# Kernel optimization log

Hardware: AMD Instinct MI355X
Metric: run time of the kernel (lower is better)

Reference implementation:

```python
import jax, jax.numpy as jnp
import numpy as np

B, N, C = 64, 1024, 128
H1, H2 = 256, 128
ACTION = N


def _xavier(key, shape):
    lim = float(np.sqrt(6.0 / (shape[0] + shape[1])))
    return jax.random.uniform(key, shape, jnp.float32, -lim, lim)


def setup_inputs() -> dict:
    key = jax.random.key(0)
    ks = jax.random.split(key, 16)
    node_features = jax.random.normal(ks[0], (B, N, 3), jnp.float32)
    adjacency_matrix = jax.random.randint(ks[1], (B, N, N), 0, 2).astype(jnp.int32)
    return {
        "node_features": node_features,
        "adjacency_matrix": adjacency_matrix,
        "W_in": _xavier(ks[2], (3, C)),
        "a_src": _xavier(ks[3], (C, 1)),
        "a_dst": _xavier(ks[4], (C, 1)),
        "a_src2": _xavier(ks[5], (C, 1)),
        "a_dst2": _xavier(ks[6], (C, 1)),
        "W1": _xavier(ks[7], (C, H1)),
        "b1": jnp.zeros((H1,), jnp.float32),
        "W2": _xavier(ks[8], (H1, H2)),
        "b2": jnp.zeros((H2,), jnp.float32),
        "Wpi": _xavier(ks[9], (H2, ACTION)),
        "bpi": jnp.zeros((ACTION,), jnp.float32),
        "Wv": _xavier(ks[10], (H2, 1)),
        "bv": jnp.zeros((1,), jnp.float32),
    }


def _gat_layer(x, mask, a_src, a_dst):
    # x: [B,N,C]; mask: [B,N,N] bool
    ai = jnp.squeeze(x @ a_src, -1)  # [B,N] score of node as source (i)
    aj = jnp.squeeze(x @ a_dst, -1)  # [B,N] score of node as dest (j)
    e = ai[:, :, None] + aj[:, None, :]  # [B,N,N]
    e = jnp.where(e > 0, e, 0.2 * e)  # leaky_relu(0.2)
    e = jnp.where(mask, e, jnp.float32(-1e9))  # masked_fill(-inf)
    alpha = jax.nn.softmax(e, axis=-1)  # [B,N,N]
    out = jnp.einsum("bij,bjc->bic", alpha, x)  # weighted neighbor aggregation
    return jax.nn.relu(out)


def reference(node_features, adjacency_matrix, W_in, a_src, a_dst, a_src2, a_dst2,
              W1, b1, W2, b2, Wpi, bpi, Wv, bv):
    mask = adjacency_matrix > 0
    x = node_features @ W_in  # [B,N,C], no bias
    x = _gat_layer(x, mask, a_src, a_dst)
    x = _gat_layer(x, mask, a_src2, a_dst2)
    x = jnp.mean(x, axis=1)  # [B,C]
    x = jax.nn.relu(x @ W1 + b1)
    x = jax.nn.relu(x @ W2 + b2)
    pi = jax.nn.softmax(x @ Wpi + bpi, axis=1)
    v = x @ Wv + bv
    return (pi, v)
```

## Files before the change

### kernel.cpp

```cpp
#include <hip/hip_runtime.h>

#define Bn 64
#define Nn 1024
#define Cc 128

typedef _Float16 h8 __attribute__((ext_vector_type(8)));
typedef float f4v __attribute__((ext_vector_type(4)));
typedef unsigned long long u64;

__global__ __launch_bounds__(256) void k_feat(
    const float* __restrict__ nf, const float* __restrict__ Win,
    const float* __restrict__ asrc, const float* __restrict__ adst,
    _Float16* __restrict__ X0, float* __restrict__ ai, float* __restrict__ aj,
    float* __restrict__ E, float* __restrict__ G, float* __restrict__ F, float* __restrict__ H) {
  int g = blockIdx.x; int b = g >> 7; int n0 = (g & 127) << 3;
  int t = threadIdx.x; int c = t >> 1; int h = t & 1;
  float w0 = Win[c], w1 = Win[Cc + c], w2 = Win[2 * Cc + c];
  float as_ = asrc[c], ad = adst[c];
  float ps[4], pd[4];
  _Float16 hv[4];
  #pragma unroll
  for (int r = 0; r < 4; r++) {
    int n = n0 + (h << 2) + r;
    const float* p = nf + ((size_t)(b << 10) + n) * 3;
    float x = p[0] * w0 + p[1] * w1 + p[2] * w2;
    hv[r] = (_Float16)x; ps[r] = x * as_; pd[r] = x * ad;
  }
  *(uint2*)(X0 + ((size_t)b << 17) + ((size_t)(g & 127) << 10) + (c << 3) + (h << 2)) = *(uint2*)hv;
  #pragma unroll
  for (int off = 32; off > 1; off >>= 1) {
    #pragma unroll
    for (int r = 0; r < 4; r++) { ps[r] += __shfl_down(ps[r], off, 64); pd[r] += __shfl_down(pd[r], off, 64); }
  }
  __shared__ float red[4][2][4][2];
  int lane = t & 63, wv = t >> 6;
  if (lane < 2) {
    #pragma unroll
    for (int r = 0; r < 4; r++) { red[wv][lane][r][0] = ps[r]; red[wv][lane][r][1] = pd[r]; }
  }
  __syncthreads();
  if (t < 8) {
    int hh = t >> 2, r = t & 3;
    float sa = 0.f, sd = 0.f;
    #pragma unroll
    for (int w = 0; w < 4; w++) { sa += red[w][hh][r][0]; sd += red[w][hh][r][1]; }
    int gi = (b << 10) + n0 + t;
    ai[gi] = sa; aj[gi] = sd;
    E[gi] = __expf(sa); G[gi] = __expf(0.2f * sa);
    F[gi] = __expf(sd); H[gi] = __expf(0.2f * sd);
  }
}

__global__ __launch_bounds__(256) void k_scores2(
    const _Float16* __restrict__ X1,
    const float* __restrict__ asrc, const float* __restrict__ adst,
    float* __restrict__ ai, float* __restrict__ aj,
    float* __restrict__ E, float* __restrict__ G, float* __restrict__ F, float* __restrict__ H) {
  int g = blockIdx.x; int b = g >> 7; int n0 = (g & 127) << 3;
  int t = threadIdx.x; int c = t >> 1; int h = t & 1;
  float as_ = asrc[c], ad = adst[c];
  uint2 raw = *(const uint2*)(X1 + ((size_t)b << 17) + ((size_t)(g & 127) << 10) + (c << 3) + (h << 2));
  const _Float16* hp = (const _Float16*)&raw;
  float ps[4], pd[4];
  #pragma unroll
  for (int r = 0; r < 4; r++) { float x = (float)hp[r]; ps[r] = x * as_; pd[r] = x * ad; }
  #pragma unroll
  for (int off = 32; off > 1; off >>= 1) {
    #pragma unroll
    for (int r = 0; r < 4; r++) { ps[r] += __shfl_down(ps[r], off, 64); pd[r] += __shfl_down(pd[r], off, 64); }
  }
  __shared__ float red[4][2][4][2];
  int lane = t & 63, wv = t >> 6;
  if (lane < 2) {
    #pragma unroll
    for (int r = 0; r < 4; r++) { red[wv][lane][r][0] = ps[r]; red[wv][lane][r][1] = pd[r]; }
  }
  __syncthreads();
  if (t < 8) {
    int hh = t >> 2, r = t & 3;
    float sa = 0.f, sd = 0.f;
    #pragma unroll
    for (int w = 0; w < 4; w++) { sa += red[w][hh][r][0]; sd += red[w][hh][r][1]; }
    int gi = (b << 10) + n0 + t;
    ai[gi] = sa; aj[gi] = sd;
    E[gi] = __expf(sa); G[gi] = __expf(0.2f * sa);
    F[gi] = __expf(sd); H[gi] = __expf(0.2f * sd);
  }
}

template <int LAYER>
__global__ __launch_bounds__(256, 3) void k_agg(
    const _Float16* __restrict__ X, const int* __restrict__ adj,
    const float* __restrict__ ai, const float* __restrict__ E, const float* __restrict__ G,
    const float* __restrict__ aj, const float* __restrict__ F, const float* __restrict__ H,
    u64* __restrict__ pm, _Float16* __restrict__ Y, float* __restrict__ xmp) {
  __shared__ __align__(16) char smem[24064];
  float* s_aj = (float*)smem;
  float* s_F  = (float*)(smem + 4096);
  float* s_H  = (float*)(smem + 8192);
  unsigned char* s_pm = (unsigned char*)(smem + 12288);
  float* s_col = (float*)(smem + 22016);

  const int b = blockIdx.y, i0 = blockIdx.x << 6;
  const int tid = threadIdx.x;
  const int lane = tid & 63, w = tid >> 6;
  const int m = lane & 15, quad = lane >> 4;
  const int gbase = b << 10;

  ((float4*)s_aj)[tid] = ((const float4*)(aj + gbase))[tid];
  ((float4*)s_F)[tid]  = ((const float4*)(F + gbase))[tid];
  ((float4*)s_H)[tid]  = ((const float4*)(H + gbase))[tid];

  if (LAYER == 1) {
    ushort* pmu = (ushort*)pm;
    #pragma unroll 2
    for (int pass = 0; pass < 16; ++pass) {
      int r = (w << 4) + pass;
      const uint4* arow = (const uint4*)(adj + ((size_t)(gbase + i0 + r) << 10));
      uint4 v0 = arow[(lane << 2) | 0], v1 = arow[(lane << 2) | 1];
      uint4 v2 = arow[(lane << 2) | 2], v3 = arow[(lane << 2) | 3];
      unsigned int bits =
          (v0.x) | (v0.y << 1) | (v0.z << 2) | (v0.w << 3) |
          (v1.x << 4) | (v1.y << 5) | (v1.z << 6) | (v1.w << 7) |
          (v2.x << 8) | (v2.y << 9) | (v2.z << 10) | (v2.w << 11) |
          (v3.x << 12) | (v3.y << 13) | (v3.z << 14) | (v3.w << 15);
      *(ushort*)(s_pm + r * 152 + (lane << 1)) = (ushort)bits;
      pmu[((size_t)(gbase + i0 + r) << 6) + lane] = (ushort)bits;
    }
  } else {
    const u64* pmg = pm + (((size_t)(gbase + i0)) << 4);
    #pragma unroll
    for (int k = tid; k < 1024; k += 256) {
      int r = k >> 4, wd = k & 15;
      *(u64*)(s_pm + r * 152 + (wd << 3)) = pmg[k];
    }
  }

  const int irow = (w << 4) + m;
  const int gi = gbase + i0 + irow;
  const float ai_i = ai[gi];
  const float Ed = E[gi], Gd = G[gi];
  float dsum = 0.f;

  f4v acc[8];
  #pragma unroll
  for (int ct = 0; ct < 8; ct++) { f4v z = {0.f, 0.f, 0.f, 0.f}; acc[ct] = z; }

  const h8* xb = (const h8*)(X + ((size_t)b << 17));
  const int prow = irow * 152;
  __syncthreads();

  for (int kt = 0; kt < 32; ++kt) {
    const h8* bsrc = xb + (kt << 9) + (quad << 7) + m;
    h8 bf0 = bsrc[0],  bf1 = bsrc[16], bf2 = bsrc[32],  bf3 = bsrc[48];
    h8 bf4 = bsrc[64], bf5 = bsrc[80], bf6 = bsrc[96],  bf7 = bsrc[112];
    const int j0 = (kt << 5) + (quad << 3);
    float aw[8], fw[8], hw[8];
    *(float4*)&aw[0] = *(const float4*)&s_aj[j0]; *(float4*)&aw[4] = *(const float4*)&s_aj[j0 + 4];
    *(float4*)&fw[0] = *(const float4*)&s_F[j0];  *(float4*)&fw[4] = *(const float4*)&s_F[j0 + 4];
    *(float4*)&hw[0] = *(const float4*)&s_H[j0];  *(float4*)&hw[4] = *(const float4*)&s_H[j0 + 4];
    unsigned int mb = s_pm[prow + (kt << 2) + quad];
    h8 af;
    #pragma unroll
    for (int jj = 0; jj < 8; jj++) {
      float e = ai_i + aw[jj];
      bool pos = e > 0.f;
      float wi_ = pos ? Ed : Gd;
      float wj_ = pos ? fw[jj] : hw[jj];
      float val = ((mb >> jj) & 1u) ? wi_ * wj_ : 0.f;
      dsum += val;
      af[jj] = (_Float16)val;
    }
    acc[0] = __builtin_amdgcn_mfma_f32_16x16x32_f16(af, bf0, acc[0], 0, 0, 0);
    acc[1] = __builtin_amdgcn_mfma_f32_16x16x32_f16(af, bf1, acc[1], 0, 0, 0);
    acc[2] = __builtin_amdgcn_mfma_f32_16x16x32_f16(af, bf2, acc[2], 0, 0, 0);
    acc[3] = __builtin_amdgcn_mfma_f32_16x16x32_f16(af, bf3, acc[3], 0, 0, 0);
    acc[4] = __builtin_amdgcn_mfma_f32_16x16x32_f16(af, bf4, acc[4], 0, 0, 0);
    acc[5] = __builtin_amdgcn_mfma_f32_16x16x32_f16(af, bf5, acc[5], 0, 0, 0);
    acc[6] = __builtin_amdgcn_mfma_f32_16x16x32_f16(af, bf6, acc[6], 0, 0, 0);
    acc[7] = __builtin_amdgcn_mfma_f32_16x16x32_f16(af, bf7, acc[7], 0, 0, 0);
  }

  dsum += __shfl_xor(dsum, 16, 64);
  dsum += __shfl_xor(dsum, 32, 64);
  float rd[4];
  #pragma unroll
  for (int r = 0; r < 4; r++) rd[r] = 1.0f / __shfl(dsum, (quad << 2) + r, 64);

  if (LAYER == 1) {
    const int g8 = ((i0 + (w << 4)) >> 3) + (quad >> 1);
    _Float16* yb = Y + ((size_t)b << 17) + (size_t)g8 * 1024 + ((quad & 1) << 2);
    #pragma unroll
    for (int ct = 0; ct < 8; ct++) {
      int c = (ct << 4) + m;
      _Float16 hv[4];
      #pragma unroll
      for (int r = 0; r < 4; r++) hv[r] = (_Float16)fmaxf(acc[ct][r] * rd[r], 0.f);
      *(uint2*)(yb + c * 8) = *(uint2*)hv;
    }
  } else {
    #pragma unroll
    for (int ct = 0; ct < 8; ct++) {
      float cs = (fmaxf(acc[ct][0] * rd[0], 0.f) + fmaxf(acc[ct][1] * rd[1], 0.f))
               + (fmaxf(acc[ct][2] * rd[2], 0.f) + fmaxf(acc[ct][3] * rd[3], 0.f));
      cs += __shfl_xor(cs, 16, 64);
      cs += __shfl_xor(cs, 32, 64);
      if (quad == 0) s_col[(w << 7) + (ct << 4) + m] = cs;
    }
    __syncthreads();
    if (tid < 128) {
      float s = s_col[tid] + s_col[128 + tid] + s_col[256 + tid] + s_col[384 + tid];
      xmp[(((b << 4) + blockIdx.x) << 7) + tid] = s;
    }
  }
}

__global__ __launch_bounds__(256) void k_head(
    const float* __restrict__ xmp, const float* __restrict__ W1, const float* __restrict__ b1,
    const float* __restrict__ W2, const float* __restrict__ b2,
    const float* __restrict__ Wpi, const float* __restrict__ bpi,
    const float* __restrict__ Wv, const float* __restrict__ bv,
    float* __restrict__ out) {
  int b = blockIdx.x, t = threadIdx.x;
  __shared__ float xs[128], h1[256], h2[128], red[4];
  if (t < 128) {
    const float* p = xmp + ((size_t)b << 11);
    float s = 0.f;
    #pragma unroll
    for (int xb = 0; xb < 16; xb++) s += p[(xb << 7) + t];
    xs[t] = s * (1.f / 1024.f);
  }
  __syncthreads();
  float s = 0.f;
  #pragma unroll 8
  for (int k = 0; k < 128; k++) s += xs[k] * W1[k * 256 + t];
  h1[t] = fmaxf(s + b1[t], 0.f);
  __syncthreads();
  if (t < 128) {
    float s2 = 0.f;
    #pragma unroll 8
    for (int k = 0; k < 256; k++) s2 += h1[k] * W2[k * 128 + t];
    h2[t] = fmaxf(s2 + b2[t], 0.f);
  }
  __syncthreads();
  float lg[4];
  #pragma unroll
  for (int q = 0; q < 4; q++) {
    int o = t + (q << 8);
    float s3 = 0.f;
    #pragma unroll 8
    for (int k = 0; k < 128; k++) s3 += h2[k] * Wpi[k * 1024 + o];
    lg[q] = s3 + bpi[o];
  }
  float mx = fmaxf(fmaxf(lg[0], lg[1]), fmaxf(lg[2], lg[3]));
  #pragma unroll
  for (int off = 32; off > 0; off >>= 1) mx = fmaxf(mx, __shfl_down(mx, off, 64));
  if ((t & 63) == 0) red[t >> 6] = mx;
  __syncthreads();
  mx = fmaxf(fmaxf(red[0], red[1]), fmaxf(red[2], red[3]));
  __syncthreads();
  float ex[4]; float sum = 0.f;
  #pragma unroll
  for (int q = 0; q < 4; q++) { ex[q] = __expf(lg[q] - mx); sum += ex[q]; }
  #pragma unroll
  for (int off = 32; off > 0; off >>= 1) sum += __shfl_down(sum, off, 64);
  if ((t & 63) == 0) red[t >> 6] = sum;
  __syncthreads();
  sum = red[0] + red[1] + red[2] + red[3];
  float rs = 1.0f / sum;
  #pragma unroll
  for (int q = 0; q < 4; q++) out[((size_t)b << 10) + t + (q << 8)] = ex[q] * rs;
  __syncthreads();
  float vp = (t < 128) ? h2[t] * Wv[t] : 0.f;
  #pragma unroll
  for (int off = 32; off > 0; off >>= 1) vp += __shfl_down(vp, off, 64);
  if ((t & 63) == 0) red[t >> 6] = vp;
  __syncthreads();
  if (t == 0) out[65536 + b] = red[0] + red[1] + red[2] + red[3] + bv[0];
}

extern "C" void kernel_launch(void* const* d_in, const int* in_sizes, int n_in,
                              void* d_out, int out_size, void* d_ws, size_t ws_size,
                              hipStream_t stream) {
  const float* nf    = (const float*)d_in[0];
  const int*   adj   = (const int*)  d_in[1];
  const float* Win   = (const float*)d_in[2];
  const float* asrc  = (const float*)d_in[3];
  const float* adst  = (const float*)d_in[4];
  const float* asrc2 = (const float*)d_in[5];
  const float* adst2 = (const float*)d_in[6];
  const float* W1    = (const float*)d_in[7];
  const float* b1    = (const float*)d_in[8];
  const float* W2    = (const float*)d_in[9];
  const float* b2    = (const float*)d_in[10];
  const float* Wpi   = (const float*)d_in[11];
  const float* bpi   = (const float*)d_in[12];
  const float* Wv    = (const float*)d_in[13];
  const float* bv    = (const float*)d_in[14];
  float* out = (float*)d_out;

  char* ws = (char*)d_ws;
  _Float16* x0 = (_Float16*)(ws);
  _Float16* x1 = (_Float16*)(ws + 16777216);
  u64* pm = (u64*)(ws + 33554432);
  char* S = ws + 41943040;
  float* ai1 = (float*)(S + 0 * 262144);
  float* aj1 = (float*)(S + 1 * 262144);
  float* E1  = (float*)(S + 2 * 262144);
  float* G1  = (float*)(S + 3 * 262144);
  float* F1  = (float*)(S + 4 * 262144);
  float* H1  = (float*)(S + 5 * 262144);
  float* ai2 = (float*)(S + 6 * 262144);
  float* aj2 = (float*)(S + 7 * 262144);
  float* E2  = (float*)(S + 8 * 262144);
  float* G2  = (float*)(S + 9 * 262144);
  float* F2  = (float*)(S + 10 * 262144);
  float* H2  = (float*)(S + 11 * 262144);
  float* xmp = (float*)(S + 12 * 262144);

  k_feat<<<8192, 256, 0, stream>>>(nf, Win, asrc, adst, x0, ai1, aj1, E1, G1, F1, H1);
  dim3 ag(16, Bn);
  k_agg<1><<<ag, 256, 0, stream>>>(x0, adj, ai1, E1, G1, aj1, F1, H1, pm, x1, nullptr);
  k_scores2<<<8192, 256, 0, stream>>>(x1, asrc2, adst2, ai2, aj2, E2, G2, F2, H2);
  k_agg<2><<<ag, 256, 0, stream>>>(x1, nullptr, ai2, E2, G2, aj2, F2, H2, pm, nullptr, xmp);
  k_head<<<Bn, 256, 0, stream>>>(xmp, W1, b1, W2, b2, Wpi, bpi, Wv, bv, out);
}
```

Baseline: 564.9 us.

## Fuse all stages into one cooperative persistent kernel with grid syncs

Replaces the five separate kernel launches with a single cooperative persistent kernel. Each stage runs as a grid-stride loop over its work items, and the stages are separated by grid.sync(). If the cooperative launch fails, the code falls back to the original five-launch sequence. The aim is to remove launch gaps and tail effects between stages. The cost is grid-wide barriers, reduced occupancy because the grid size comes from an occupancy query, and the loss of the launch_bounds(256,3) hint on the aggregation stage. The adjacency packing loop unroll also goes from 2 to 4.

```diff
diff --git a/kernel.cpp b/kernel.cpp
--- a/kernel.cpp
+++ b/kernel.cpp
@@ -1,4 +1,7 @@
 #include <hip/hip_runtime.h>
+#include <hip/hip_cooperative_groups.h>
+
+namespace cg = cooperative_groups;
 
 #define Bn 64
 #define Nn 1024
@@ -8,13 +11,28 @@
 typedef float f4v __attribute__((ext_vector_type(4)));
 typedef unsigned long long u64;
 
-__global__ __launch_bounds__(256) void k_feat(
-    const float* __restrict__ nf, const float* __restrict__ Win,
+struct Params {
+  const float* nf; const int* adj;
+  const float* Win; const float* asrc; const float* adst;
+  const float* asrc2; const float* adst2;
+  const float* W1; const float* b1; const float* W2; const float* b2;
+  const float* Wpi; const float* bpi; const float* Wv; const float* bv;
+  float* out;
+  _Float16* x0; _Float16* x1; u64* pm;
+  float* ai1; float* aj1; float* E1; float* G1; float* F1; float* H1;
+  float* ai2; float* aj2; float* E2; float* G2; float* F2; float* H2;
+  float* xmp;
+};
+
+__device__ __forceinline__ void feat_group(
+    int g, int t, const float* __restrict__ nf, const float* __restrict__ Win,
     const float* __restrict__ asrc, const float* __restrict__ adst,
     _Float16* __restrict__ X0, float* __restrict__ ai, float* __restrict__ aj,
-    float* __restrict__ E, float* __restrict__ G, float* __restrict__ F, float* __restrict__ H) {
-  int g = blockIdx.x; int b = g >> 7; int n0 = (g & 127) << 3;
-  int t = threadIdx.x; int c = t >> 1; int h = t & 1;
+    float* __restrict__ E, float* __restrict__ G, float* __restrict__ F, float* __restrict__ H,
+    char* smem) {
+  float (*red)[2][4][2] = (float(*)[2][4][2])smem;
+  int b = g >> 7; int n0 = (g & 127) << 3;
+  int c = t >> 1; int h = t & 1;
   float w0 = Win[c], w1 = Win[Cc + c], w2 = Win[2 * Cc + c];
   float as_ = asrc[c], ad = adst[c];
   float ps[4], pd[4];
@@ -32,7 +50,6 @@
     #pragma unroll
     for (int r = 0; r < 4; r++) { ps[r] += __shfl_down(ps[r], off, 64); pd[r] += __shfl_down(pd[r], off, 64); }
   }
-  __shared__ float red[4][2][4][2];
   int lane = t & 63, wv = t >> 6;
   if (lane < 2) {
     #pragma unroll
@@ -49,15 +66,18 @@
     E[gi] = __expf(sa); G[gi] = __expf(0.2f * sa);
     F[gi] = __expf(sd); H[gi] = __expf(0.2f * sd);
   }
-}
-
-__global__ __launch_bounds__(256) void k_scores2(
-    const _Float16* __restrict__ X1,
+  __syncthreads();
+}
+
+__device__ __forceinline__ void scores_group(
+    int g, int t, const _Float16* __restrict__ X1,
     const float* __restrict__ asrc, const float* __restrict__ adst,
     float* __restrict__ ai, float* __restrict__ aj,
-    float* __restrict__ E, float* __restrict__ G, float* __restrict__ F, float* __restrict__ H) {
-  int g = blockIdx.x; int b = g >> 7; int n0 = (g & 127) << 3;
-  int t = threadIdx.x; int c = t >> 1; int h = t & 1;
+    float* __restrict__ E, float* __restrict__ G, float* __restrict__ F, float* __restrict__ H,
+    char* smem) {
+  float (*red)[2][4][2] = (float(*)[2][4][2])smem;
+  int b = g >> 7; int n0 = (g & 127) << 3;
+  int c = t >> 1; int h = t & 1;
   float as_ = asrc[c], ad = adst[c];
   uint2 raw = *(const uint2*)(X1 + ((size_t)b << 17) + ((size_t)(g & 127) << 10) + (c << 3) + (h << 2));
   const _Float16* hp = (const _Float16*)&raw;
@@ -69,7 +89,6 @@
     #pragma unroll
     for (int r = 0; r < 4; r++) { ps[r] += __shfl_down(ps[r], off, 64); pd[r] += __shfl_down(pd[r], off, 64); }
   }
-  __shared__ float red[4][2][4][2];
   int lane = t & 63, wv = t >> 6;
   if (lane < 2) {
     #pragma unroll
@@ -86,34 +105,36 @@
     E[gi] = __expf(sa); G[gi] = __expf(0.2f * sa);
     F[gi] = __expf(sd); H[gi] = __expf(0.2f * sd);
   }
+  __syncthreads();
 }
 
 template <int LAYER>
-__global__ __launch_bounds__(256, 3) void k_agg(
+__device__ __forceinline__ void agg_tile(
+    int b, int i0, char* smem,
     const _Float16* __restrict__ X, const int* __restrict__ adj,
     const float* __restrict__ ai, const float* __restrict__ E, const float* __restrict__ G,
     const float* __restrict__ aj, const float* __restrict__ F, const float* __restrict__ H,
-    u64* __restrict__ pm, _Float16* __restrict__ Y, float* __restrict__ xmp) {
-  __shared__ __align__(16) char smem[24064];
+    u64* __restrict__ pm, _Float16* __restrict__ Y, float* __restrict__ xmp, int xslot) {
   float* s_aj = (float*)smem;
   float* s_F  = (float*)(smem + 4096);
   float* s_H  = (float*)(smem + 8192);
   unsigned char* s_pm = (unsigned char*)(smem + 12288);
   float* s_col = (float*)(smem + 22016);
 
-  const int b = blockIdx.y, i0 = blockIdx.x << 6;
   const int tid = threadIdx.x;
   const int lane = tid & 63, w = tid >> 6;
   const int m = lane & 15, quad = lane >> 4;
   const int gbase = b << 10;
 
+  __syncthreads();
+
   ((float4*)s_aj)[tid] = ((const float4*)(aj + gbase))[tid];
   ((float4*)s_F)[tid]  = ((const float4*)(F + gbase))[tid];
   ((float4*)s_H)[tid]  = ((const float4*)(H + gbase))[tid];
 
   if (LAYER == 1) {
     ushort* pmu = (ushort*)pm;
-    #pragma unroll 2
+    #pragma unroll 4
     for (int pass = 0; pass < 16; ++pass) {
       int r = (w << 4) + pass;
       const uint4* arow = (const uint4*)(adj + ((size_t)(gbase + i0 + r) << 10));
@@ -210,19 +231,23 @@
     __syncthreads();
     if (tid < 128) {
       float s = s_col[tid] + s_col[128 + tid] + s_col[256 + tid] + s_col[384 + tid];
-      xmp[(((b << 4) + blockIdx.x) << 7) + tid] = s;
-    }
-  }
-}
-
-__global__ __launch_bounds__(256) void k_head(
-    const float* __restrict__ xmp, const float* __restrict__ W1, const float* __restrict__ b1,
+      xmp[(xslot << 7) + tid] = s;
+    }
+  }
+}
+
+__device__ __forceinline__ void head_batch(
+    int b, int t, char* smem, const float* __restrict__ xmp,
+    const float* __restrict__ W1, const float* __restrict__ b1,
     const float* __restrict__ W2, const float* __restrict__ b2,
     const float* __restrict__ Wpi, const float* __restrict__ bpi,
     const float* __restrict__ Wv, const float* __restrict__ bv,
     float* __restrict__ out) {
-  int b = blockIdx.x, t = threadIdx.x;
-  __shared__ float xs[128], h1[256], h2[128], red[4];
+  float* xs = (float*)smem;
+  float* h1 = xs + 128;
+  float* h2 = h1 + 256;
+  float* red = h2 + 128;
+  __syncthreads();
   if (t < 128) {
     const float* p = xmp + ((size_t)b << 11);
     float s = 0.f;
@@ -279,49 +304,118 @@
   if (t == 0) out[65536 + b] = red[0] + red[1] + red[2] + red[3] + bv[0];
 }
 
+__global__ __launch_bounds__(256) void mega(Params p) {
+  __shared__ __align__(16) char smem[24064];
+  cg::grid_group grid = cg::this_grid();
+  const int bid = blockIdx.x;
+  const int nb = gridDim.x;
+  const int t = threadIdx.x;
+
+  for (int g = bid; g < 8192; g += nb)
+    feat_group(g, t, p.nf, p.Win, p.asrc, p.adst,
+               p.x0, p.ai1, p.aj1, p.E1, p.G1, p.F1, p.H1, smem);
+  grid.sync();
+
+  for (int tile = bid; tile < 1024; tile += nb)
+    agg_tile<1>(tile >> 4, (tile & 15) << 6, smem, p.x0, p.adj,
+                p.ai1, p.E1, p.G1, p.aj1, p.F1, p.H1, p.pm, p.x1, nullptr, 0);
+  grid.sync();
+
+  for (int g = bid; g < 8192; g += nb)
+    scores_group(g, t, p.x1, p.asrc2, p.adst2,
+                 p.ai2, p.aj2, p.E2, p.G2, p.F2, p.H2, smem);
+  grid.sync();
+
+  for (int tile = bid; tile < 1024; tile += nb)
+    agg_tile<2>(tile >> 4, (tile & 15) << 6, smem, p.x1, nullptr,
+                p.ai2, p.E2, p.G2, p.aj2, p.F2, p.H2, p.pm, nullptr, p.xmp, tile);
+  grid.sync();
+
+  for (int b = bid; b < Bn; b += nb)
+    head_batch(b, t, smem, p.xmp, p.W1, p.b1, p.W2, p.b2,
+               p.Wpi, p.bpi, p.Wv, p.bv, p.out);
+}
+
+__global__ __launch_bounds__(256) void k_feat_w(Params p) {
+  __shared__ __align__(16) char smem[24064];
+  feat_group(blockIdx.x, threadIdx.x, p.nf, p.Win, p.asrc, p.adst,
+             p.x0, p.ai1, p.aj1, p.E1, p.G1, p.F1, p.H1, smem);
+}
+__global__ __launch_bounds__(256, 3) void k_agg1_w(Params p) {
+  __shared__ __align__(16) char smem[24064];
+  agg_tile<1>(blockIdx.y, blockIdx.x << 6, smem, p.x0, p.adj,
+              p.ai1, p.E1, p.G1, p.aj1, p.F1, p.H1, p.pm, p.x1, nullptr, 0);
+}
+__global__ __launch_bounds__(256) void k_scores_w(Params p) {
+  __shared__ __align__(16) char smem[24064];
+  scores_group(blockIdx.x, threadIdx.x, p.x1, p.asrc2, p.adst2,
+               p.ai2, p.aj2, p.E2, p.G2, p.F2, p.H2, smem);
+}
+__global__ __launch_bounds__(256, 3) void k_agg2_w(Params p) {
+  __shared__ __align__(16) char smem[24064];
+  agg_tile<2>(blockIdx.y, blockIdx.x << 6, smem, p.x1, nullptr,
+              p.ai2, p.E2, p.G2, p.aj2, p.F2, p.H2, p.pm, nullptr, p.xmp,
+              ((int)blockIdx.y << 4) + blockIdx.x);
+}
+__global__ __launch_bounds__(256) void k_head_w(Params p) {
+  __shared__ __align__(16) char smem[24064];
+  head_batch(blockIdx.x, threadIdx.x, smem, p.xmp, p.W1, p.b1, p.W2, p.b2,
+             p.Wpi, p.bpi, p.Wv, p.bv, p.out);
+}
+
 extern "C" void kernel_launch(void* const* d_in, const int* in_sizes, int n_in,
                               void* d_out, int out_size, void* d_ws, size_t ws_size,
                               hipStream_t stream) {
-  const float* nf    = (const float*)d_in[0];
-  const int*   adj   = (const int*)  d_in[1];
-  const float* Win   = (const float*)d_in[2];
-  const float* asrc  = (const float*)d_in[3];
-  const float* adst  = (const float*)d_in[4];
-  const float* asrc2 = (const float*)d_in[5];
-  const float* adst2 = (const float*)d_in[6];
-  const float* W1    = (const float*)d_in[7];
-  const float* b1    = (const float*)d_in[8];
-  const float* W2    = (const float*)d_in[9];
-  const float* b2    = (const float*)d_in[10];
-  const float* Wpi   = (const float*)d_in[11];
-  const float* bpi   = (const float*)d_in[12];
-  const float* Wv    = (const float*)d_in[13];
-  const float* bv    = (const float*)d_in[14];
-  float* out = (float*)d_out;
-
   char* ws = (char*)d_ws;
-  _Float16* x0 = (_Float16*)(ws);
-  _Float16* x1 = (_Float16*)(ws + 16777216);
-  u64* pm = (u64*)(ws + 33554432);
+  Params p;
+  p.nf    = (const float*)d_in[0];
+  p.adj   = (const int*)  d_in[1];
+  p.Win   = (const float*)d_in[2];
+  p.asrc  = (const float*)d_in[3];
+  p.adst  = (const float*)d_in[4];
+  p.asrc2 = (const float*)d_in[5];
+  p.adst2 = (const float*)d_in[6];
+  p.W1    = (const float*)d_in[7];
+  p.b1    = (const float*)d_in[8];
+  p.W2    = (const float*)d_in[9];
+  p.b2    = (const float*)d_in[10];
+  p.Wpi   = (const float*)d_in[11];
+  p.bpi   = (const float*)d_in[12];
+  p.Wv    = (const float*)d_in[13];
+  p.bv    = (const float*)d_in[14];
+  p.out   = (float*)d_out;
+  p.x0 = (_Float16*)(ws);
+  p.x1 = (_Float16*)(ws + 16777216);
+  p.pm = (u64*)(ws + 33554432);
   char* S = ws + 41943040;
-  float* ai1 = (float*)(S + 0 * 262144);
-  float* aj1 = (float*)(S + 1 * 262144);
-  float* E1  = (float*)(S + 2 * 262144);
-  float* G1  = (float*)(S + 3 * 262144);
-  float* F1  = (float*)(S + 4 * 262144);
-  float* H1  = (float*)(S + 5 * 262144);
-  float* ai2 = (float*)(S + 6 * 262144);
-  float* aj2 = (float*)(S + 7 * 262144);
-  float* E2  = (float*)(S + 8 * 262144);
-  float* G2  = (float*)(S + 9 * 262144);
-  float* F2  = (float*)(S + 10 * 262144);
-  float* H2  = (float*)(S + 11 * 262144);
-  float* xmp = (float*)(S + 12 * 262144);
-
-  k_feat<<<8192, 256, 0, stream>>>(nf, Win, asrc, adst, x0, ai1, aj1, E1, G1, F1, H1);
-  dim3 ag(16, Bn);
-  k_agg<1><<<ag, 256, 0, stream>>>(x0, adj, ai1, E1, G1, aj1, F1, H1, pm, x1, nullptr);
-  k_scores2<<<8192, 256, 0, stream>>>(x1, asrc2, adst2, ai2, aj2, E2, G2, F2, H2);
-  k_agg<2><<<ag, 256, 0, stream>>>(x1, nullptr, ai2, E2, G2, aj2, F2, H2, pm, nullptr, xmp);
-  k_head<<<Bn, 256, 0, stream>>>(xmp, W1, b1, W2, b2, Wpi, bpi, Wv, bv, out);
-}
+  p.ai1 = (float*)(S + 0 * 262144);
+  p.aj1 = (float*)(S + 1 * 262144);
+  p.E1  = (float*)(S + 2 * 262144);
+  p.G1  = (float*)(S + 3 * 262144);
+  p.F1  = (float*)(S + 4 * 262144);
+  p.H1  = (float*)(S + 5 * 262144);
+  p.ai2 = (float*)(S + 6 * 262144);
+  p.aj2 = (float*)(S + 7 * 262144);
+  p.E2  = (float*)(S + 8 * 262144);
+  p.G2  = (float*)(S + 9 * 262144);
+  p.F2  = (float*)(S + 10 * 262144);
+  p.H2  = (float*)(S + 11 * 262144);
+  p.xmp = (float*)(S + 12 * 262144);
+
+  int mb = 0;
+  hipError_t qerr = hipOccupancyMaxActiveBlocksPerMultiprocessor(&mb, mega, 256, 0);
+  if (qerr != hipSuccess || mb < 1) mb = 1;
+  if (mb > 4) mb = 4;
+  int nb = mb * 256;
+  if (nb > 1024) nb = 1024;
+
+  void* kargs[] = { (void*)&p };
+  hipError_t err = hipLaunchCooperativeKernel(mega, dim3(nb), dim3(256), kargs, 0, stream);
+  if (err != hipSuccess) {
+    k_feat_w<<<8192, 256, 0, stream>>>(p);
+    k_agg1_w<<<dim3(16, Bn), 256, 0, stream>>>(p);
+    k_scores_w<<<8192, 256, 0, stream>>>(p);
+    k_agg2_w<<<dim3(16, Bn), 256, 0, stream>>>(p);
+    k_head_w<<<Bn, 256, 0, stream>>>(p);
+  }
+}
```

New measurement: 732.7 us. +29.7%, slower.
